# Kernel tuning notes

Measured on AMD Instinct MI355X. Metric: run time of the kernel, lower is better.

## Reference

```python
import jax, jax.numpy as jnp
import numpy as np

B, S, D, H = 2, 4096, 256, 8
P = 64               # proj_dim_l
R = S // P           # proj_dim_r = 64, P*R == S
DH = D // H          # head_dim = 32


def setup_inputs() -> dict:
    key = jax.random.key(0)
    kx, kl, kr, kv, ko = jax.random.split(key, 5)
    scale = 0.05  # stand-in for xavier-uniform scale
    x  = jax.random.normal(kx, (B, S, D), dtype=jnp.float32)
    Wl = jax.random.normal(kl, (D, P), dtype=jnp.float32) * scale
    Wr = jax.random.normal(kr, (D, R), dtype=jnp.float32) * scale
    Wv = jax.random.normal(kv, (D, D), dtype=jnp.float32) * scale
    Wo = jax.random.normal(ko, (D, D), dtype=jnp.float32) * scale
    return {"x": x, "Wl": Wl, "Wr": Wr, "Wv": Wv, "Wo": Wo}


def reference(x, Wl, Wr, Wv, Wo):
    b, s, d = x.shape
    # value projection + head split -> (b, H, S, DH). Dropout p=0 (eval) = identity.
    v = (x @ Wv).reshape(b, s, H, DH).transpose(0, 2, 1, 3)
    # factorized score: row n is vec(outer(l_n, r_n)) of length P*R == S
    l = x @ Wl                                   # (b, S, P)
    r = x @ Wr                                   # (b, S, R)
    attn = (l[:, :, :, None] * r[:, :, None, :]).reshape(b, s, s)  # (b, S, S)
    score = jax.nn.softmax(attn, axis=-1)        # (b, S, S)
    # shared score across heads, per-head value matmul
    o = jnp.einsum('bnm,bhmd->bhnd', score, v)   # (b, H, S, DH)
    o = o.transpose(0, 2, 1, 3).reshape(b, s, d) # concat heads
    return o @ Wo
```

## Files before the change

kernel.cpp:

```cpp
#include <hip/hip_runtime.h>
#include <hip/hip_bf16.h>

typedef __attribute__((ext_vector_type(8))) __bf16 bf16x8;
typedef __attribute__((ext_vector_type(4))) __bf16 bf16x4;
typedef __attribute__((ext_vector_type(4))) float  f32x4;

#define MFMA16(a, b, c) __builtin_amdgcn_mfma_f32_16x16x32_bf16((a), (b), (c), 0, 0, 0)

static constexpr size_t OFF_WVT  = 0;
static constexpr size_t OFF_WLT  = OFF_WVT + 256 * 256 * 2;
static constexpr size_t OFF_WRT  = OFF_WLT + 64 * 256 * 2;
static constexpr size_t OFF_VT   = 1u << 20;
static constexpr size_t OFF_L    = 6u << 20;
static constexpr size_t OFF_R    = 8u << 20;
static constexpr size_t OFF_PART = 10u << 20;
static constexpr size_t OFF_ZP   = 26u << 20;

__device__ __forceinline__ float fast_exp2(float x) {
  float e;
  asm("v_exp_f32 %0, %1" : "=v"(e) : "v"(x));
  return e;
}

__device__ __forceinline__ bf16x8 cvt8(float4 a, float4 b) {
  bf16x8 o;
  o[0] = (__bf16)a.x; o[1] = (__bf16)a.y; o[2] = (__bf16)a.z; o[3] = (__bf16)a.w;
  o[4] = (__bf16)b.x; o[5] = (__bf16)b.y; o[6] = (__bf16)b.z; o[7] = (__bf16)b.w;
  return o;
}

__device__ __forceinline__ void gll16(const __bf16* g, __bf16* l) {
  __builtin_amdgcn_global_load_lds((const __attribute__((address_space(1))) void*)g,
                                   (__attribute__((address_space(3))) void*)l,
                                   16, 0, 0);
}

__global__ __launch_bounds__(256) void k_prepw(const float* __restrict__ Wv,
                                               const float* __restrict__ Wl,
                                               const float* __restrict__ Wr,
                                               const float* __restrict__ Wo,
                                               __bf16* __restrict__ Wvt,
                                               __bf16* __restrict__ Wlt,
                                               __bf16* __restrict__ Wrt) {
  const int blk = blockIdx.x;
  const int t = threadIdx.x;
  if (blk < 128) {
    const int idx = blk * 256 + t;
    if (idx < 16384) {
      const int k = idx >> 6, n = idx & 63;
      Wlt[n * 256 + k] = (__bf16)Wl[idx];
    } else {
      const int j = idx - 16384;
      const int k = j >> 6, n = j & 63;
      Wrt[n * 256 + k] = (__bf16)Wr[j];
    }
  } else {
    const int k = blk - 128;
    const int n = t;
    const float* wvr = Wv + (size_t)k * 256;
    float a0 = 0.f, a1 = 0.f, a2 = 0.f, a3 = 0.f;
#pragma unroll 4
    for (int j = 0; j < 256; j += 4) {
      a0 += wvr[j + 0] * Wo[(size_t)(j + 0) * 256 + n];
      a1 += wvr[j + 1] * Wo[(size_t)(j + 1) * 256 + n];
      a2 += wvr[j + 2] * Wo[(size_t)(j + 2) * 256 + n];
      a3 += wvr[j + 3] * Wo[(size_t)(j + 3) * 256 + n];
    }
    Wvt[(size_t)n * 256 + k] = (__bf16)((a0 + a1) + (a2 + a3));
  }
}

__global__ __launch_bounds__(256) void k_proj(const float* __restrict__ x,
                                              const __bf16* __restrict__ Wvt,
                                              const __bf16* __restrict__ Wlt,
                                              const __bf16* __restrict__ Wrt,
                                              __bf16* __restrict__ Vt,
                                              float* __restrict__ lbuf,
                                              float* __restrict__ rbuf) {
  __shared__ __align__(16) __bf16 vs[8 * 64 * 8];
  const int t = threadIdx.x;
  const int lane = t & 63, wave = t >> 6;
  const int l16 = lane & 15, quad = lane >> 4;
  const int wr = wave >> 1, wc = wave & 1;
  const int rbk = blockIdx.x;
  const int ct  = blockIdx.y;
  const __bf16* Wt;
  int colbase;
  if (ct < 4)       { Wt = Wvt; colbase = ct * 64; }
  else if (ct == 4) { Wt = Wlt; colbase = 0; }
  else              { Wt = Wrt; colbase = 0; }
  const int row0 = rbk * 64 + wr * 32;
  const int c0   = colbase + wc * 32;
  f32x4 acc[2][2] = {};
  for (int kk = 0; kk < 256; kk += 32) {
    const int ko = kk + quad * 8;
    const float* xr0 = x + (size_t)(row0 + l16) * 256 + ko;
    const float* xr1 = x + (size_t)(row0 + 16 + l16) * 256 + ko;
    bf16x8 a0 = cvt8(*(const float4*)xr0, *(const float4*)(xr0 + 4));
    bf16x8 a1 = cvt8(*(const float4*)xr1, *(const float4*)(xr1 + 4));
    bf16x8 b0 = *(const bf16x8*)(Wt + (size_t)(c0 + l16) * 256 + ko);
    bf16x8 b1 = *(const bf16x8*)(Wt + (size_t)(c0 + 16 + l16) * 256 + ko);
    acc[0][0] = MFMA16(a0, b0, acc[0][0]);
    acc[0][1] = MFMA16(a0, b1, acc[0][1]);
    acc[1][0] = MFMA16(a1, b0, acc[1][0]);
    acc[1][1] = MFMA16(a1, b1, acc[1][1]);
  }
  if (ct < 4) {
#pragma unroll
    for (int mt = 0; mt < 2; ++mt)
#pragma unroll
      for (int nt = 0; nt < 2; ++nt) {
        const int m8 = wr * 4 + mt * 2 + (quad >> 1);
        const int d  = wc * 32 + nt * 16 + l16;
        bf16x4 o;
        o.x = (__bf16)acc[mt][nt][0];
        o.y = (__bf16)acc[mt][nt][1];
        o.z = (__bf16)acc[mt][nt][2];
        o.w = (__bf16)acc[mt][nt][3];
        *(bf16x4*)(&vs[m8 * 512 + d * 8 + (quad & 1) * 4]) = o;
      }
    __syncthreads();
    const int m8 = t >> 5, s32 = t & 31;
    const int bat = rbk >> 6, mc = rbk & 63;
    bf16x8 a = *(const bf16x8*)(&vs[m8 * 512 + s32 * 16]);
    bf16x8 b = *(const bf16x8*)(&vs[m8 * 512 + s32 * 16 + 8]);
    __bf16* dst = Vt + (size_t)bat * 1048576 + (size_t)mc * 16384 +
                  m8 * 2048 + ct * 512 + s32 * 16;
    *(bf16x8*)dst       = a;
    *(bf16x8*)(dst + 8) = b;
  } else {
    float* dstb = (ct == 4) ? lbuf : rbuf;
#pragma unroll
    for (int mt = 0; mt < 2; ++mt)
#pragma unroll
      for (int nt = 0; nt < 2; ++nt) {
        const int col = c0 + nt * 16 + l16;
        const int gr  = rbk * 64 + wr * 32 + mt * 16 + quad * 4;
#pragma unroll
        for (int rr = 0; rr < 4; ++rr)
          dstb[(size_t)(gr + rr) * 64 + col] = acc[mt][nt][rr];
      }
  }
}

__global__ __launch_bounds__(512, 2) void k_attn(const float* __restrict__ lbuf,
                                                 const float* __restrict__ rbuf,
                                                 const __bf16* __restrict__ Vt,
                                                 __bf16* __restrict__ part,
                                                 float* __restrict__ zpart) {
  __shared__ __align__(16) char smem[74240];
  __bf16* vt0 = (__bf16*)smem;
  __bf16* vt1 = (__bf16*)(smem + 32768);
  float*  ls  = (float*)(smem + 65536);
  const int t = threadIdx.x;
  const int lane = t & 63, w = t >> 6;
  const int l16 = lane & 15, quad = lane >> 4;
  const int wr = w >> 1, wc = w & 1;
  const int rb = blockIdx.x;
  const int sp = blockIdx.y;
  const int g0 = rb * 128;
  const int bat = rb >> 5;
  const __bf16* Vbase = Vt + (size_t)bat * 1048576;
  const int ck0 = sp * 16;

  {
    const int idx = t * 4;
    const int row = idx >> 4, c = idx & 15;
    f32x4 v = *(const f32x4*)(lbuf + (size_t)(g0 + row) * 64 + ck0 + c);
    ls[row * 17 + c + 0] = v[0];
    ls[row * 17 + c + 1] = v[1];
    ls[row * 17 + c + 2] = v[2];
    ls[row * 17 + c + 3] = v[3];
  }
  const float LOG2E = 1.44269504088896f;
  float rreg[2][16];
#pragma unroll
  for (int mt = 0; mt < 2; ++mt) {
    const float* rp = rbuf + (size_t)(g0 + wr * 32 + mt * 16 + l16) * 64;
    f32x4 a = *(const f32x4*)(rp + quad * 8);
    f32x4 b = *(const f32x4*)(rp + quad * 8 + 4);
    f32x4 c = *(const f32x4*)(rp + 32 + quad * 8);
    f32x4 d = *(const f32x4*)(rp + 32 + quad * 8 + 4);
#pragma unroll
    for (int j = 0; j < 4; ++j) {
      rreg[mt][j]      = a[j] * LOG2E;
      rreg[mt][4 + j]  = b[j] * LOG2E;
      rreg[mt][8 + j]  = c[j] * LOG2E;
      rreg[mt][12 + j] = d[j] * LOG2E;
    }
  }

  f32x4 acc[2][8] = {};
  float zacc[2] = {0.f, 0.f};

  {
    const __bf16* src = Vbase + (size_t)ck0 * 16384;
#pragma unroll
    for (int i = 0; i < 4; ++i)
      gll16(src + (size_t)(i * 512 + t) * 8, vt0 + (i * 512 + (w << 6)) * 8);
  }
  __syncthreads();

  for (int kc = 0; kc < 16; ++kc) {
    __bf16* cur = (kc & 1) ? vt1 : vt0;
    __bf16* nxt = (kc & 1) ? vt0 : vt1;
    if (kc < 15) {
      const __bf16* src = Vbase + (size_t)(ck0 + kc + 1) * 16384;
#pragma unroll
      for (int i = 0; i < 4; ++i)
        gll16(src + (size_t)(i * 512 + t) * 8, nxt + (i * 512 + (w << 6)) * 8);
    }
    bf16x8 af[2][2];
#pragma unroll
    for (int mt = 0; mt < 2; ++mt) {
      const float lv = ls[(wr * 32 + mt * 16 + l16) * 17 + kc];
#pragma unroll
      for (int kk = 0; kk < 2; ++kk)
#pragma unroll
        for (int j = 0; j < 8; ++j) {
          const float e = fast_exp2(lv * rreg[mt][kk * 8 + j]);
          zacc[mt] += e;
          af[mt][kk][j] = (__bf16)e;
        }
    }
#pragma unroll
    for (int kk = 0; kk < 2; ++kk)
#pragma unroll
      for (int nt = 0; nt < 8; ++nt) {
        bf16x8 bv = *(const bf16x8*)(cur + (kk * 4 + quad) * 2048 +
                                     (wc * 128 + nt * 16 + l16) * 8);
        acc[0][nt] = MFMA16(af[0][kk], bv, acc[0][nt]);
        acc[1][nt] = MFMA16(af[1][kk], bv, acc[1][nt]);
      }
    __syncthreads();
  }

#pragma unroll
  for (int mt = 0; mt < 2; ++mt) {
    float z = zacc[mt];
    z += __shfl_xor(z, 16);
    z += __shfl_xor(z, 32);
    if (wc == 0 && quad == 0)
      zpart[(size_t)sp * 8192 + g0 + wr * 32 + mt * 16 + l16] = z;
  }

  __bf16* ctile = (__bf16*)smem;
#pragma unroll
  for (int mt = 0; mt < 2; ++mt)
#pragma unroll
    for (int nt = 0; nt < 8; ++nt) {
      const int r0 = wr * 32 + mt * 16 + quad * 4;
      const int c  = wc * 128 + nt * 16 + l16;
#pragma unroll
      for (int rr = 0; rr < 4; ++rr)
        ctile[(r0 + rr) * 264 + c] = (__bf16)acc[mt][nt][rr];
    }
  __syncthreads();
  __bf16* pb = part + (size_t)sp * (8192 * 256);
#pragma unroll
  for (int p = 0; p < 8; ++p) {
    const int u = p * 512 + t;
    const int row = u >> 5, seg = u & 31;
    *(bf16x8*)(pb + (size_t)(g0 + row) * 256 + seg * 8) =
        *(const bf16x8*)(ctile + row * 264 + seg * 8);
  }
}

__global__ __launch_bounds__(256) void k_fix(const __bf16* __restrict__ part,
                                             const float* __restrict__ zpart,
                                             float* __restrict__ out) {
  const int idx = blockIdx.x * 256 + threadIdx.x;
  const int g = idx >> 5, seg = idx & 31;
  float z = 0.f;
#pragma unroll
  for (int s = 0; s < 4; ++s) z += zpart[(size_t)s * 8192 + g];
  const float iz = 1.0f / z;
  float sum[8] = {};
#pragma unroll
  for (int s = 0; s < 4; ++s) {
    bf16x8 p = *(const bf16x8*)(part + (size_t)s * (8192 * 256) + (size_t)g * 256 + seg * 8);
#pragma unroll
    for (int j = 0; j < 8; ++j) sum[j] += (float)p[j];
  }
  f32x4 o0, o1;
#pragma unroll
  for (int j = 0; j < 4; ++j) { o0[j] = sum[j] * iz; o1[j] = sum[4 + j] * iz; }
  float* dst = out + (size_t)g * 256 + seg * 8;
  *(f32x4*)dst       = o0;
  *(f32x4*)(dst + 4) = o1;
}

extern "C" void kernel_launch(void* const* d_in, const int* in_sizes, int n_in,
                              void* d_out, int out_size, void* d_ws, size_t ws_size,
                              hipStream_t stream) {
  const float* x  = (const float*)d_in[0];
  const float* Wl = (const float*)d_in[1];
  const float* Wr = (const float*)d_in[2];
  const float* Wv = (const float*)d_in[3];
  const float* Wo = (const float*)d_in[4];
  char* ws = (char*)d_ws;
  __bf16* Wvt = (__bf16*)(ws + OFF_WVT);
  __bf16* Wlt = (__bf16*)(ws + OFF_WLT);
  __bf16* Wrt = (__bf16*)(ws + OFF_WRT);
  __bf16* Vt  = (__bf16*)(ws + OFF_VT);
  float*  lb  = (float*)(ws + OFF_L);
  float*  rbf = (float*)(ws + OFF_R);
  __bf16* prt = (__bf16*)(ws + OFF_PART);
  float*  zp  = (float*)(ws + OFF_ZP);
  float*  out = (float*)d_out;

  k_prepw<<<384, 256, 0, stream>>>(Wv, Wl, Wr, Wo, Wvt, Wlt, Wrt);
  k_proj<<<dim3(128, 6), 256, 0, stream>>>(x, Wvt, Wlt, Wrt, Vt, lb, rbf);
  k_attn<<<dim3(64, 4), 512, 0, stream>>>(lb, rbf, Vt, prt, zp);
  k_fix<<<1024, 256, 0, stream>>>(prt, zp, out);
}
```

Measured before the change: 122.2 us.

## Software-pipeline exp computation with MFMA and remap block indices for locality

The attention loop is unrolled by two with two sets of A-fragment registers, so the exp/convert work for the next K chunk is issued before the MFMAs of the current chunk and can interleave with them. This hides transcendental latency behind matrix work. The z accumulator is split per kk to shorten the dependency chain. Both the projection and attention kernels switch to a 1-D grid with a custom block-id mapping, which groups blocks that share weight or V tiles to improve L2/MALL locality. The extra live A-fragments raise register pressure and could lower occupancy under launch_bounds(512,2).

```diff
diff --git a/kernel.cpp b/kernel.cpp
--- a/kernel.cpp
+++ b/kernel.cpp
@@ -82,8 +82,11 @@
   const int lane = t & 63, wave = t >> 6;
   const int l16 = lane & 15, quad = lane >> 4;
   const int wr = wave >> 1, wc = wave & 1;
-  const int rbk = blockIdx.x;
-  const int ct  = blockIdx.y;
+  const int bid = blockIdx.x;
+  const int q   = bid / 48;
+  const int rmd = bid - q * 48;
+  const int ct  = rmd >> 3;
+  const int rbk = q * 8 + (rmd & 7);
   const __bf16* Wt;
   int colbase;
   if (ct < 4)       { Wt = Wvt; colbase = ct * 64; }
@@ -156,10 +159,12 @@
   const int lane = t & 63, w = t >> 6;
   const int l16 = lane & 15, quad = lane >> 4;
   const int wr = w >> 1, wc = w & 1;
-  const int rb = blockIdx.x;
-  const int sp = blockIdx.y;
+  const int bid = blockIdx.x;
+  const int cmb = bid & 7;
+  const int sp  = cmb >> 1;
+  const int bat = cmb & 1;
+  const int rb  = bat * 32 + (bid >> 3);
   const int g0 = rb * 128;
-  const int bat = rb >> 5;
   const __bf16* Vbase = Vt + (size_t)bat * 1048576;
   const int ck0 = sp * 16;
 
@@ -191,53 +196,70 @@
   }
 
   f32x4 acc[2][8] = {};
-  float zacc[2] = {0.f, 0.f};
-
-  {
-    const __bf16* src = Vbase + (size_t)ck0 * 16384;
-#pragma unroll
-    for (int i = 0; i < 4; ++i)
-      gll16(src + (size_t)(i * 512 + t) * 8, vt0 + (i * 512 + (w << 6)) * 8);
-  }
+  float zacc[2][2] = {{0.f, 0.f}, {0.f, 0.f}};
+
+#define STAGE(KC, DST)                                                        \
+  {                                                                           \
+    const __bf16* src = Vbase + (size_t)(ck0 + (KC)) * 16384;                 \
+    _Pragma("unroll")                                                         \
+    for (int i = 0; i < 4; ++i)                                               \
+      gll16(src + (size_t)(i * 512 + t) * 8, (DST) + (i * 512 + (w << 6)) * 8); \
+  }
+
+#define AF_COMPUTE(KC, AF)                                                    \
+  {                                                                           \
+    _Pragma("unroll")                                                         \
+    for (int mt = 0; mt < 2; ++mt) {                                          \
+      const float lv = ls[(wr * 32 + mt * 16 + l16) * 17 + (KC)];             \
+      _Pragma("unroll")                                                       \
+      for (int kk = 0; kk < 2; ++kk)                                          \
+        _Pragma("unroll")                                                     \
+        for (int j = 0; j < 8; ++j) {                                         \
+          const float e = fast_exp2(lv * rreg[mt][kk * 8 + j]);               \
+          zacc[mt][kk] += e;                                                  \
+          AF[mt][kk][j] = (__bf16)e;                                          \
+        }                                                                     \
+    }                                                                         \
+  }
+
+#define MFMA_PHASE(CUR, AF)                                                   \
+  {                                                                           \
+    _Pragma("unroll")                                                         \
+    for (int kk = 0; kk < 2; ++kk)                                            \
+      _Pragma("unroll")                                                       \
+      for (int nt = 0; nt < 8; ++nt) {                                        \
+        bf16x8 bv = *(const bf16x8*)((CUR) + (kk * 4 + quad) * 2048 +         \
+                                     (wc * 128 + nt * 16 + l16) * 8);         \
+        acc[0][nt] = MFMA16(AF[0][kk], bv, acc[0][nt]);                       \
+        acc[1][nt] = MFMA16(AF[1][kk], bv, acc[1][nt]);                       \
+      }                                                                       \
+  }
+
+  STAGE(0, vt0);
   __syncthreads();
-
-  for (int kc = 0; kc < 16; ++kc) {
-    __bf16* cur = (kc & 1) ? vt1 : vt0;
-    __bf16* nxt = (kc & 1) ? vt0 : vt1;
-    if (kc < 15) {
-      const __bf16* src = Vbase + (size_t)(ck0 + kc + 1) * 16384;
-#pragma unroll
-      for (int i = 0; i < 4; ++i)
-        gll16(src + (size_t)(i * 512 + t) * 8, nxt + (i * 512 + (w << 6)) * 8);
-    }
-    bf16x8 af[2][2];
-#pragma unroll
-    for (int mt = 0; mt < 2; ++mt) {
-      const float lv = ls[(wr * 32 + mt * 16 + l16) * 17 + kc];
-#pragma unroll
-      for (int kk = 0; kk < 2; ++kk)
-#pragma unroll
-        for (int j = 0; j < 8; ++j) {
-          const float e = fast_exp2(lv * rreg[mt][kk * 8 + j]);
-          zacc[mt] += e;
-          af[mt][kk][j] = (__bf16)e;
-        }
-    }
-#pragma unroll
-    for (int kk = 0; kk < 2; ++kk)
-#pragma unroll
-      for (int nt = 0; nt < 8; ++nt) {
-        bf16x8 bv = *(const bf16x8*)(cur + (kk * 4 + quad) * 2048 +
-                                     (wc * 128 + nt * 16 + l16) * 8);
-        acc[0][nt] = MFMA16(af[0][kk], bv, acc[0][nt]);
-        acc[1][nt] = MFMA16(af[1][kk], bv, acc[1][nt]);
-      }
+  bf16x8 afA[2][2], afB[2][2];
+  AF_COMPUTE(0, afA);
+
+  for (int kc = 0; kc < 16; kc += 2) {
+    STAGE(kc + 1, vt1);
+    AF_COMPUTE(kc + 1, afB);
+    MFMA_PHASE(vt0, afA);
     __syncthreads();
-  }
+    if (kc + 2 < 16) {
+      STAGE(kc + 2, vt0);
+      AF_COMPUTE(kc + 2, afA);
+    }
+    MFMA_PHASE(vt1, afB);
+    __syncthreads();
+  }
+
+#undef STAGE
+#undef AF_COMPUTE
+#undef MFMA_PHASE
 
 #pragma unroll
   for (int mt = 0; mt < 2; ++mt) {
-    float z = zacc[mt];
+    float z = zacc[mt][0] + zacc[mt][1];
     z += __shfl_xor(z, 16);
     z += __shfl_xor(z, 32);
     if (wc == 0 && quad == 0)
@@ -310,7 +332,7 @@
   float*  out = (float*)d_out;
 
   k_prepw<<<384, 256, 0, stream>>>(Wv, Wl, Wr, Wo, Wvt, Wlt, Wrt);
-  k_proj<<<dim3(128, 6), 256, 0, stream>>>(x, Wvt, Wlt, Wrt, Vt, lb, rbf);
-  k_attn<<<dim3(64, 4), 512, 0, stream>>>(lb, rbf, Vt, prt, zp);
+  k_proj<<<768, 256, 0, stream>>>(x, Wvt, Wlt, Wrt, Vt, lb, rbf);
+  k_attn<<<256, 512, 0, stream>>>(lb, rbf, Vt, prt, zp);
   k_fix<<<1024, 256, 0, stream>>>(prt, zp, out);
 }
```

Measured after the change: 121.7 us. Within noise of the previous version (-0.5%).

## Retile attention into smaller 64-row, 128-column blocks with direct V loads

Applied to the files above, without the earlier changes.

The attention kernel now uses 256-thread blocks covering 64 rows and half the output columns, launched as 1024 blocks instead of 256, so the grid fills all CUs. The LDS double buffer filled with global_load_lds is replaced by direct per-lane global loads of V fragments, which removes the per-chunk barriers but recomputes the exponentials twice (once per column half) and relies on cache for V reuse. The projection kernel's grid is flattened and remapped so blocks sharing rows are scheduled together. Block IDs are also interleaved over split and batch to spread work.

```diff
diff --git a/kernel.cpp b/kernel.cpp
--- a/kernel.cpp
+++ b/kernel.cpp
@@ -27,12 +27,6 @@
   o[0] = (__bf16)a.x; o[1] = (__bf16)a.y; o[2] = (__bf16)a.z; o[3] = (__bf16)a.w;
   o[4] = (__bf16)b.x; o[5] = (__bf16)b.y; o[6] = (__bf16)b.z; o[7] = (__bf16)b.w;
   return o;
-}
-
-__device__ __forceinline__ void gll16(const __bf16* g, __bf16* l) {
-  __builtin_amdgcn_global_load_lds((const __attribute__((address_space(1))) void*)g,
-                                   (__attribute__((address_space(3))) void*)l,
-                                   16, 0, 0);
 }
 
 __global__ __launch_bounds__(256) void k_prepw(const float* __restrict__ Wv,
@@ -82,8 +76,11 @@
   const int lane = t & 63, wave = t >> 6;
   const int l16 = lane & 15, quad = lane >> 4;
   const int wr = wave >> 1, wc = wave & 1;
-  const int rbk = blockIdx.x;
-  const int ct  = blockIdx.y;
+  const int bid = blockIdx.x;
+  const int q   = bid / 48;
+  const int rmd = bid - q * 48;
+  const int ct  = rmd >> 3;
+  const int rbk = q * 8 + (rmd & 7);
   const __bf16* Wt;
   int colbase;
   if (ct < 4)       { Wt = Wvt; colbase = ct * 64; }
@@ -143,29 +140,31 @@
   }
 }
 
-__global__ __launch_bounds__(512, 2) void k_attn(const float* __restrict__ lbuf,
+__global__ __launch_bounds__(256, 4) void k_attn(const float* __restrict__ lbuf,
                                                  const float* __restrict__ rbuf,
                                                  const __bf16* __restrict__ Vt,
                                                  __bf16* __restrict__ part,
                                                  float* __restrict__ zpart) {
-  __shared__ __align__(16) char smem[74240];
-  __bf16* vt0 = (__bf16*)smem;
-  __bf16* vt1 = (__bf16*)(smem + 32768);
-  float*  ls  = (float*)(smem + 65536);
+  __shared__ __align__(16) char smem[17408];
+  float* ls = (float*)smem;
   const int t = threadIdx.x;
   const int lane = t & 63, w = t >> 6;
   const int l16 = lane & 15, quad = lane >> 4;
   const int wr = w >> 1, wc = w & 1;
-  const int rb = blockIdx.x;
-  const int sp = blockIdx.y;
-  const int g0 = rb * 128;
-  const int bat = rb >> 5;
+  const int bid = blockIdx.x;
+  const int cmb = bid & 7;
+  const int sp  = cmb >> 1;
+  const int bat = cmb & 1;
+  const int u   = bid >> 3;
+  const int ch  = u >> 6;
+  const int rbl = u & 63;
+  const int g0 = bat * 4096 + rbl * 64;
+  const int cbase = ch * 128;
   const __bf16* Vbase = Vt + (size_t)bat * 1048576;
   const int ck0 = sp * 16;
 
   {
-    const int idx = t * 4;
-    const int row = idx >> 4, c = idx & 15;
+    const int row = t >> 2, c = (t & 3) * 4;
     f32x4 v = *(const f32x4*)(lbuf + (size_t)(g0 + row) * 64 + ck0 + c);
     ls[row * 17 + c + 0] = v[0];
     ls[row * 17 + c + 1] = v[1];
@@ -189,27 +188,20 @@
       rreg[mt][12 + j] = d[j] * LOG2E;
     }
   }
-
-  f32x4 acc[2][8] = {};
-  float zacc[2] = {0.f, 0.f};
-
-  {
-    const __bf16* src = Vbase + (size_t)ck0 * 16384;
-#pragma unroll
-    for (int i = 0; i < 4; ++i)
-      gll16(src + (size_t)(i * 512 + t) * 8, vt0 + (i * 512 + (w << 6)) * 8);
-  }
   __syncthreads();
 
+  f32x4 acc[2][4] = {};
+  float zacc[2][2] = {{0.f, 0.f}, {0.f, 0.f}};
+
   for (int kc = 0; kc < 16; ++kc) {
-    __bf16* cur = (kc & 1) ? vt1 : vt0;
-    __bf16* nxt = (kc & 1) ? vt0 : vt1;
-    if (kc < 15) {
-      const __bf16* src = Vbase + (size_t)(ck0 + kc + 1) * 16384;
-#pragma unroll
-      for (int i = 0; i < 4; ++i)
-        gll16(src + (size_t)(i * 512 + t) * 8, nxt + (i * 512 + (w << 6)) * 8);
-    }
+    const __bf16* src = Vbase + (size_t)(ck0 + kc) * 16384;
+    bf16x8 bv[2][4];
+#pragma unroll
+    for (int kk = 0; kk < 2; ++kk)
+#pragma unroll
+      for (int nt = 0; nt < 4; ++nt)
+        bv[kk][nt] = *(const bf16x8*)(src + (kk * 4 + quad) * 2048 +
+                                      (cbase + wc * 64 + nt * 16 + l16) * 8);
     bf16x8 af[2][2];
 #pragma unroll
     for (int mt = 0; mt < 2; ++mt) {
@@ -219,50 +211,48 @@
 #pragma unroll
         for (int j = 0; j < 8; ++j) {
           const float e = fast_exp2(lv * rreg[mt][kk * 8 + j]);
-          zacc[mt] += e;
+          zacc[mt][kk] += e;
           af[mt][kk][j] = (__bf16)e;
         }
     }
 #pragma unroll
     for (int kk = 0; kk < 2; ++kk)
 #pragma unroll
-      for (int nt = 0; nt < 8; ++nt) {
-        bf16x8 bv = *(const bf16x8*)(cur + (kk * 4 + quad) * 2048 +
-                                     (wc * 128 + nt * 16 + l16) * 8);
-        acc[0][nt] = MFMA16(af[0][kk], bv, acc[0][nt]);
-        acc[1][nt] = MFMA16(af[1][kk], bv, acc[1][nt]);
+      for (int nt = 0; nt < 4; ++nt) {
+        acc[0][nt] = MFMA16(af[0][kk], bv[kk][nt], acc[0][nt]);
+        acc[1][nt] = MFMA16(af[1][kk], bv[kk][nt], acc[1][nt]);
       }
-    __syncthreads();
   }
 
 #pragma unroll
   for (int mt = 0; mt < 2; ++mt) {
-    float z = zacc[mt];
+    float z = zacc[mt][0] + zacc[mt][1];
     z += __shfl_xor(z, 16);
     z += __shfl_xor(z, 32);
-    if (wc == 0 && quad == 0)
+    if (wc == 0 && quad == 0 && ch == 0)
       zpart[(size_t)sp * 8192 + g0 + wr * 32 + mt * 16 + l16] = z;
   }
 
+  __syncthreads();
   __bf16* ctile = (__bf16*)smem;
 #pragma unroll
   for (int mt = 0; mt < 2; ++mt)
 #pragma unroll
-    for (int nt = 0; nt < 8; ++nt) {
+    for (int nt = 0; nt < 4; ++nt) {
       const int r0 = wr * 32 + mt * 16 + quad * 4;
-      const int c  = wc * 128 + nt * 16 + l16;
+      const int cl = wc * 64 + nt * 16 + l16;
 #pragma unroll
       for (int rr = 0; rr < 4; ++rr)
-        ctile[(r0 + rr) * 264 + c] = (__bf16)acc[mt][nt][rr];
+        ctile[(r0 + rr) * 136 + cl] = (__bf16)acc[mt][nt][rr];
     }
   __syncthreads();
   __bf16* pb = part + (size_t)sp * (8192 * 256);
 #pragma unroll
-  for (int p = 0; p < 8; ++p) {
-    const int u = p * 512 + t;
-    const int row = u >> 5, seg = u & 31;
-    *(bf16x8*)(pb + (size_t)(g0 + row) * 256 + seg * 8) =
-        *(const bf16x8*)(ctile + row * 264 + seg * 8);
+  for (int p = 0; p < 4; ++p) {
+    const int uu = p * 256 + t;
+    const int row = uu >> 4, seg = uu & 15;
+    *(bf16x8*)(pb + (size_t)(g0 + row) * 256 + cbase + seg * 8) =
+        *(const bf16x8*)(ctile + row * 136 + seg * 8);
   }
 }
 
@@ -310,7 +300,7 @@
   float*  out = (float*)d_out;
 
   k_prepw<<<384, 256, 0, stream>>>(Wv, Wl, Wr, Wo, Wvt, Wlt, Wrt);
-  k_proj<<<dim3(128, 6), 256, 0, stream>>>(x, Wvt, Wlt, Wrt, Vt, lb, rbf);
-  k_attn<<<dim3(64, 4), 512, 0, stream>>>(lb, rbf, Vt, prt, zp);
+  k_proj<<<768, 256, 0, stream>>>(x, Wvt, Wlt, Wrt, Vt, lb, rbf);
+  k_attn<<<1024, 256, 0, stream>>>(lb, rbf, Vt, prt, zp);
   k_fix<<<1024, 256, 0, stream>>>(prt, zp, out);
 }
```

New measurement: 140.4 us. 1.15x slower.
